# Optimization experiments

Hardware: AMD Instinct MI355X
Metric: run time of the kernel (lower is better)

Reference implementation:

```python
import jax, jax.numpy as jnp
import numpy as np

DIM = 1024
NUM_HEADS = 16
HEAD_DIM = DIM // NUM_HEADS


def setup_inputs() -> dict:
    key = jax.random.key(0)
    k_x, k_qkv, k_proj, k_b = jax.random.split(key, 4)
    B, N, P, C = 4, 96, 64, DIM
    x = jax.random.normal(k_x, (B, N, P, C), dtype=jnp.float32)
    # nn.Linear(dim, 3*dim, bias=False): store as (in, out) for x @ W
    s = 1.0 / np.sqrt(C)
    W_qkv = jax.random.uniform(k_qkv, (C, 3 * C), minval=-s, maxval=s, dtype=jnp.float32)
    W_proj = jax.random.uniform(k_proj, (C, C), minval=-s, maxval=s, dtype=jnp.float32)
    b_proj = jax.random.uniform(k_b, (C,), minval=-s, maxval=s, dtype=jnp.float32)
    return {"x": x, "W_qkv": W_qkv, "W_proj": W_proj, "b_proj": b_proj}


def reference(x, W_qkv, W_proj, b_proj):
    B, N, P, C = x.shape
    H, hd = NUM_HEADS, C // NUM_HEADS
    # qkv projection: (B,N,P,3C) -> (B,N,P,3,H,hd)
    qkv = (x @ W_qkv).reshape(B, N, P, 3, H, hd)
    # q,k: mean-pool over patches P -> (B,H,N,hd)
    q = qkv[..., 0, :, :].mean(axis=2).transpose(0, 2, 1, 3)
    k = qkv[..., 1, :, :].mean(axis=2).transpose(0, 2, 1, 3)
    # v keeps all patches: (B,N,P,H,hd) -> (B,H,N,hd,P) -> (B,H,N,hd*P)
    v = qkv[..., 2, :, :].transpose(0, 3, 1, 4, 2).reshape(B, H, N, hd * P)
    # SDPA with default scale 1/sqrt(q_last_dim) = 1/sqrt(hd)
    scores = jnp.einsum('bhnd,bhmd->bhnm', q, k) * (hd ** -0.5)
    attn = jax.nn.softmax(scores, axis=-1)
    out = jnp.einsum('bhnm,bhme->bhne', attn, v)  # e = hd*P
    # unflatten back to (B,N,P,C)
    out = out.reshape(B, H, N, hd, P).transpose(0, 2, 4, 1, 3).reshape(B, N, P, C)
    return out @ W_proj + b_proj
```

## Files before the change

kernel.cpp:

```cpp
#include <hip/hip_runtime.h>
#include <cstdint>
#include <cstddef>

#define PPP  64
#define CC   1024

typedef __attribute__((ext_vector_type(8))) short short8;
typedef __attribute__((ext_vector_type(4))) float floatx4;
typedef __attribute__((ext_vector_type(4))) unsigned short ushort4v;

__device__ inline float bf2f(unsigned short u) {
  union { unsigned int i; float f; } v; v.i = ((unsigned int)u) << 16; return v.f;
}
__device__ inline unsigned short f2bf(float f) {
  union { float f; unsigned int i; } v; v.f = f;
  unsigned int x = v.i;
  unsigned int r = (x + 0x7fffu + ((x >> 16) & 1u)) >> 16;
  return (unsigned short)r;
}

#define GLD16(gp, lp)                                                          \
  __builtin_amdgcn_global_load_lds(                                            \
      (const __attribute__((address_space(1))) void*)(gp),                     \
      (__attribute__((address_space(3))) void*)(lp), 16, 0, 0)

__global__ __launch_bounds__(256) void conv_mean(
    const float* __restrict__ x, unsigned short* __restrict__ xbf,
    unsigned short* __restrict__ xm) {
  int bn = blockIdx.x;
  int c4 = threadIdx.x * 4;
  const float* xp = x + (size_t)bn * (PPP * CC) + c4;
  unsigned short* xo = xbf + (size_t)bn * (PPP * CC) + c4;
  float4 s = {0.f, 0.f, 0.f, 0.f};
#pragma unroll 8
  for (int p = 0; p < PPP; ++p) {
    float4 v = *(const float4*)&xp[(size_t)p * CC];
    s.x += v.x; s.y += v.y; s.z += v.z; s.w += v.w;
    ushort4v pk;
    pk.x = f2bf(v.x); pk.y = f2bf(v.y); pk.z = f2bf(v.z); pk.w = f2bf(v.w);
    *(ushort4v*)&xo[(size_t)p * CC] = pk;
  }
  ushort4v pm;
  pm.x = f2bf(s.x * (1.0f / PPP)); pm.y = f2bf(s.y * (1.0f / PPP));
  pm.z = f2bf(s.z * (1.0f / PPP)); pm.w = f2bf(s.w * (1.0f / PPP));
  *(ushort4v*)&xm[(size_t)bn * CC + c4] = pm;
}

__global__ __launch_bounds__(256) void transpose_f32_bf16(
    const float* __restrict__ src, unsigned short* __restrict__ dst,
    int R, int Cc, int src_stride) {
  __shared__ unsigned short tile[32][33];
  int tc = blockIdx.x * 32, tr = blockIdx.y * 32;
  int tx = threadIdx.x & 31, ty = threadIdx.x >> 5;
  for (int yy = ty; yy < 32; yy += 8)
    tile[yy][tx] = f2bf(src[(size_t)(tr + yy) * src_stride + tc + tx]);
  __syncthreads();
  for (int yy = ty; yy < 32; yy += 8)
    dst[(size_t)(tc + yy) * R + tr + tx] = tile[tx][yy];
}

template <bool F32OUT, bool SWIZ>
__global__ __launch_bounds__(256) void gemm_bt(
    const unsigned short* __restrict__ A, const unsigned short* __restrict__ BT,
    void* __restrict__ Cout, const float* __restrict__ bias,
    int M, int N, int K, int nbx) {
  __shared__ unsigned short As[128 * 32];
  __shared__ unsigned short Bs[128 * 32];

  int bx, by;
  {
    int bid = blockIdx.x;
    if (SWIZ) {
      bx = (bid >> 3) & 7;
      by = (bid & 7) * (gridDim.x >> 6) + (bid >> 6);
    } else {
      bx = bid % nbx;
      by = bid / nbx;
    }
  }
  const int rowBase = by * 128;
  const int colBase = bx * 128;
  const int t = threadIdx.x;
  const int wave = t >> 6, lane = t & 63;
  const int qr = wave >> 1, qc = wave & 1;
  const int m16 = lane & 15, quad = lane >> 4;

  floatx4 acc[4][4];
#pragma unroll
  for (int i = 0; i < 4; ++i)
#pragma unroll
    for (int j = 0; j < 4; ++j) {
      acc[i][j][0] = 0.f; acc[i][j][1] = 0.f; acc[i][j][2] = 0.f; acc[i][j][3] = 0.f;
    }

  for (int k0 = 0; k0 < K; k0 += 32) {
    __syncthreads();
#pragma unroll
    for (int u = 0; u < 2; ++u) {
      int ch = (u * 4 + wave) * 64 + lane;
      int row = ch >> 2, c8 = (ch & 3) << 3;
      GLD16(&A [(size_t)(rowBase + row) * K + k0 + c8], &As[ch * 8]);
      GLD16(&BT[(size_t)(colBase + row) * K + k0 + c8], &Bs[ch * 8]);
    }
    __syncthreads();

    short8 af[4], bfr[4];
#pragma unroll
    for (int i = 0; i < 4; ++i)
      af[i] = *(const short8*)&As[(qr * 64 + i * 16 + m16) * 32 + quad * 8];
#pragma unroll
    for (int j = 0; j < 4; ++j)
      bfr[j] = *(const short8*)&Bs[(qc * 64 + j * 16 + m16) * 32 + quad * 8];
#pragma unroll
    for (int i = 0; i < 4; ++i)
#pragma unroll
      for (int j = 0; j < 4; ++j)
        acc[i][j] = __builtin_amdgcn_mfma_f32_16x16x32_bf16(af[i], bfr[j], acc[i][j], 0, 0, 0);
  }

  float bv[4];
#pragma unroll
  for (int j = 0; j < 4; ++j)
    bv[j] = bias ? bias[colBase + qc * 64 + j * 16 + m16] : 0.f;

#pragma unroll
  for (int i = 0; i < 4; ++i) {
    int row0 = rowBase + qr * 64 + i * 16 + quad * 4;
#pragma unroll
    for (int j = 0; j < 4; ++j) {
      int col = colBase + qc * 64 + j * 16 + m16;
#pragma unroll
      for (int r = 0; r < 4; ++r) {
        float f = acc[i][j][r] + bv[j];
        if (F32OUT)
          ((float*)Cout)[(size_t)(row0 + r) * N + col] = f;
        else
          ((unsigned short*)Cout)[(size_t)(row0 + r) * N + col] = f2bf(f);
      }
    }
  }
}

template <bool F32OUT>
__global__ __launch_bounds__(512, 2) void gemm_bt256(
    const unsigned short* __restrict__ A, const unsigned short* __restrict__ BT,
    void* __restrict__ Cout, const float* __restrict__ bias,
    int M, int N, int K) {
  __shared__ __attribute__((aligned(16))) unsigned short As[2][256 * 64];
  __shared__ __attribute__((aligned(16))) unsigned short Bs[3][256 * 64];

  const int nbx = N >> 8;
  int tid = (blockIdx.x & 7) * (gridDim.x >> 3) + (blockIdx.x >> 3);
  const int bx = tid % nbx, by = tid / nbx;
  const int rowBase = by * 256, colBase = bx * 256;

  const int t = threadIdx.x;
  const int wave = t >> 6, lane = t & 63;
  const int wr = wave >> 2, wc = wave & 3;
  const int m16 = lane & 15, quad = lane >> 4;
  const int sw7 = m16 & 7;

  const unsigned short* srcA[4];
  int offA[4];
#pragma unroll
  for (int u = 0; u < 4; ++u) {
    int c = u * 512 + t;
    int row = c >> 3, pch = c & 7;
    int l = pch ^ (row & 7);
    srcA[u] = A + (size_t)(rowBase + row) * K + l * 8;
    offA[u] = c * 8;
  }
  const unsigned short* srcB[2][2];
  int offB[2][2];
#pragma unroll
  for (int g = 0; g < 2; ++g)
#pragma unroll
    for (int u = 0; u < 2; ++u) {
      int i = u * 512 + t;
      int col = g * 32 + ((i >> 8) << 6) + ((i >> 3) & 31);
      int kcp = i & 7;
      int l = kcp ^ (col & 7);
      srcB[g][u] = BT + (size_t)(colBase + col) * K + l * 8;
      offB[g][u] = col * 64 + kcp * 8;
    }

  floatx4 acc[8][4];
#pragma unroll
  for (int i = 0; i < 8; ++i)
#pragma unroll
    for (int j = 0; j < 4; ++j) {
      acc[i][j][0] = 0.f; acc[i][j][1] = 0.f; acc[i][j][2] = 0.f; acc[i][j][3] = 0.f;
    }

  short8 ar[4][2];
  short8 br[2][2][2];

#define RD_A(buf, qa)                                                          \
  _Pragma("unroll") for (int i_ = 0; i_ < 4; ++i_)                             \
  _Pragma("unroll") for (int kh_ = 0; kh_ < 2; ++kh_)                          \
    ar[i_][kh_] = *(const short8*)&As[buf][                                    \
        (wr * 128 + (qa) * 64 + i_ * 16 + m16) * 64 +                          \
        (((kh_ * 4 + quad) ^ sw7) * 8)];
#define RD_B(buf, qb)                                                          \
  _Pragma("unroll") for (int j_ = 0; j_ < 2; ++j_)                             \
  _Pragma("unroll") for (int kh_ = 0; kh_ < 2; ++kh_)                          \
    br[qb][j_][kh_] = *(const short8*)&Bs[buf][                                \
        (wc * 64 + (qb) * 32 + j_ * 16 + m16) * 64 +                           \
        (((kh_ * 4 + quad) ^ sw7) * 8)];
#define MFMA_PH(qa, qb)                                                        \
  __builtin_amdgcn_s_setprio(1);                                               \
  _Pragma("unroll") for (int kh_ = 0; kh_ < 2; ++kh_)                          \
  _Pragma("unroll") for (int i_ = 0; i_ < 4; ++i_)                             \
  _Pragma("unroll") for (int j_ = 0; j_ < 2; ++j_)                             \
    acc[(qa) * 4 + i_][(qb) * 2 + j_] =                                        \
        __builtin_amdgcn_mfma_f32_16x16x32_bf16(                               \
            ar[i_][kh_], br[qb][j_][kh_], acc[(qa) * 4 + i_][(qb) * 2 + j_],   \
            0, 0, 0);                                                          \
  __builtin_amdgcn_s_setprio(0);
#define WAITV(n) asm volatile("s_waitcnt vmcnt(" #n ")" ::: "memory")
#define BARR() asm volatile("s_barrier" ::: "memory")
#define FEN() asm volatile("" ::: "memory")

  GLD16(srcB[0][0], &Bs[0][offB[0][0]]);
  GLD16(srcB[0][1], &Bs[0][offB[0][1]]); FEN();
  GLD16(srcB[1][0], &Bs[0][offB[1][0]]);
  GLD16(srcB[1][1], &Bs[0][offB[1][1]]); FEN();
  GLD16(srcA[0], &As[0][offA[0]]);
  GLD16(srcA[2], &As[0][offA[2]]); FEN();
  GLD16(srcA[1], &As[0][offA[1]]);
  GLD16(srcA[3], &As[0][offA[3]]); FEN();
  GLD16(srcB[0][0] + 64, &Bs[1][offB[0][0]]);
  GLD16(srcB[0][1] + 64, &Bs[1][offB[0][1]]); FEN();
  GLD16(srcB[1][0] + 64, &Bs[1][offB[1][0]]);
  GLD16(srcB[1][1] + 64, &Bs[1][offB[1][1]]); FEN();

  const int NT = K >> 6;
  int acur = 0, bcur = 0;
#pragma unroll 1
  for (int kt = 0; kt < NT - 1; ++kt) {
    const int anxt = acur ^ 1;
    const int bnx2 = (bcur >= 1) ? bcur - 1 : 2;
    const int koA = (kt + 1) << 6;
    const int koB = (kt + 2) << 6;
    const bool doB = (kt + 2) < NT;
    WAITV(4); BARR();
    RD_A(acur, 0);
    RD_B(bcur, 0);
    RD_B(bcur, 1);
    GLD16(srcA[0] + koA, &As[anxt][offA[0]]);
    GLD16(srcA[2] + koA, &As[anxt][offA[2]]); FEN();
    MFMA_PH(0, 0);
    GLD16(srcA[1] + koA, &As[anxt][offA[1]]);
    GLD16(srcA[3] + koA, &As[anxt][offA[3]]); FEN();
    MFMA_PH(0, 1);
    RD_A(acur, 1);
    if (doB) {
      GLD16(srcB[0][0] + koB, &Bs[bnx2][offB[0][0]]);
      GLD16(srcB[0][1] + koB, &Bs[bnx2][offB[0][1]]);
    }
    FEN();
    MFMA_PH(1, 0);
    if (doB) {
      GLD16(srcB[1][0] + koB, &Bs[bnx2][offB[1][0]]);
      GLD16(srcB[1][1] + koB, &Bs[bnx2][offB[1][1]]);
    }
    FEN();
    MFMA_PH(1, 1);
    acur = anxt; bcur = (bcur == 2) ? 0 : bcur + 1;
  }
  WAITV(0); BARR();
  RD_A(acur, 0); RD_B(bcur, 0); RD_B(bcur, 1);
  MFMA_PH(0, 0);
  MFMA_PH(0, 1);
  RD_A(acur, 1);
  MFMA_PH(1, 0);
  MFMA_PH(1, 1);

#undef RD_A
#undef RD_B
#undef MFMA_PH
#undef WAITV
#undef BARR
#undef FEN

  float bv[4];
#pragma unroll
  for (int jg = 0; jg < 4; ++jg)
    bv[jg] = bias ? bias[colBase + wc * 64 + jg * 16 + m16] : 0.f;

#pragma unroll
  for (int ig = 0; ig < 8; ++ig) {
    int row0 = rowBase + wr * 128 + ig * 16 + quad * 4;
#pragma unroll
    for (int jg = 0; jg < 4; ++jg) {
      int col = colBase + wc * 64 + jg * 16 + m16;
#pragma unroll
      for (int r = 0; r < 4; ++r) {
        float f = acc[ig][jg][r] + bv[jg];
        if (F32OUT)
          ((float*)Cout)[(size_t)(row0 + r) * N + col] = f;
        else
          ((unsigned short*)Cout)[(size_t)(row0 + r) * N + col] = f2bf(f);
      }
    }
  }
}

__global__ __launch_bounds__(128) void softmax_k(
    const float* __restrict__ qk, unsigned short* __restrict__ attn) {
  int bh = blockIdx.x;
  int b = bh >> 4, h = bh & 15;
  __shared__ float ks[96][64];
  __shared__ float sc[96][96];
  int t = threadIdx.x;
  for (int idx = t; idx < 96 * 64; idx += 128) {
    int n = idx >> 6, d = idx & 63;
    ks[n][d] = qk[(size_t)(b * 96 + n) * 2048 + 1024 + h * 64 + d];
  }
  __syncthreads();
  if (t < 96) {
    float qreg[64];
    const float* qrow = qk + (size_t)(b * 96 + t) * 2048 + h * 64;
#pragma unroll
    for (int d = 0; d < 64; ++d) qreg[d] = qrow[d];

    float mx = -1e30f;
    for (int m = 0; m < 96; ++m) {
      float s0 = 0.f, s1 = 0.f, s2 = 0.f, s3 = 0.f;
#pragma unroll
      for (int d = 0; d < 64; d += 4) {
        s0 += qreg[d + 0] * ks[m][d + 0];
        s1 += qreg[d + 1] * ks[m][d + 1];
        s2 += qreg[d + 2] * ks[m][d + 2];
        s3 += qreg[d + 3] * ks[m][d + 3];
      }
      float s = ((s0 + s1) + (s2 + s3)) * 0.125f;
      sc[m][t] = s;
      mx = fmaxf(mx, s);
    }
    float sum = 0.f;
    for (int m = 0; m < 96; ++m) {
      float e = __expf(sc[m][t] - mx);
      sc[m][t] = e;
      sum += e;
    }
    float inv = 1.0f / sum;
    size_t base = (size_t)(bh * 96 + t) * 96;
    for (int m = 0; m < 96; ++m) attn[base + m] = f2bf(sc[m][t] * inv);
  }
}

__global__ __launch_bounds__(256) void attn_apply_mfma(
    const unsigned short* __restrict__ attn, const unsigned short* __restrict__ V,
    unsigned short* __restrict__ out2) {
  const int bid = blockIdx.x;
  const int bh = bid >> 5, ct = bid & 31;
  const int b = bh >> 4;
  const int t = threadIdx.x;
  const int wave = t >> 6, lane = t & 63;
  const int m16 = lane & 15, quad = lane >> 4;

  const unsigned short* An = attn + (size_t)bh * 96 * 96;
  const int vb = b * 96 * 64 * CC;

  floatx4 acc[6][2];
#pragma unroll
  for (int i = 0; i < 6; ++i)
#pragma unroll
    for (int j = 0; j < 2; ++j) {
      acc[i][j][0] = 0.f; acc[i][j][1] = 0.f; acc[i][j][2] = 0.f; acc[i][j][3] = 0.f;
    }

  int p_[2], base_[2];
#pragma unroll
  for (int jj = 0; jj < 2; ++jj) {
    int colL = wave * 32 + jj * 16;
    int p = ct * 2 + (colL >> 6);
    int d = (colL & 63) + m16;
    p_[jj] = p;
    base_[jj] = vb + p * CC + ((bh & 15) * 64) + d;
  }

#pragma unroll
  for (int k0 = 0; k0 < 96; k0 += 32) {
    short8 af[6];
#pragma unroll
    for (int i = 0; i < 6; ++i)
      af[i] = *(const short8*)&An[(i * 16 + m16) * 96 + k0 + quad * 8];
#pragma unroll
    for (int jj = 0; jj < 2; ++jj) {
      short8 bfr;
#pragma unroll
      for (int j = 0; j < 8; ++j)
        bfr[j] = (short)V[(size_t)base_[jj] + (size_t)(k0 + quad * 8 + j) * (64 * CC)];
#pragma unroll
      for (int i = 0; i < 6; ++i)
        acc[i][jj] = __builtin_amdgcn_mfma_f32_16x16x32_bf16(af[i], bfr, acc[i][jj], 0, 0, 0);
    }
  }

#pragma unroll
  for (int jj = 0; jj < 2; ++jj) {
    int colL = wave * 32 + jj * 16;
    int d = (colL & 63) + m16;
    size_t obase = (size_t)(b * 96) * 64 * CC + (size_t)p_[jj] * CC + (bh & 15) * 64 + d;
#pragma unroll
    for (int i = 0; i < 6; ++i) {
#pragma unroll
      for (int r = 0; r < 4; ++r) {
        int n = i * 16 + quad * 4 + r;
        out2[obase + (size_t)n * (64 * CC)] = f2bf(acc[i][jj][r]);
      }
    }
  }
}

extern "C" void kernel_launch(void* const* d_in, const int* in_sizes, int n_in,
                              void* d_out, int out_size, void* d_ws, size_t ws_size,
                              hipStream_t stream) {
  const float* x      = (const float*)d_in[0];
  const float* W_qkv  = (const float*)d_in[1];
  const float* W_proj = (const float*)d_in[2];
  const float* b_proj = (const float*)d_in[3];
  float* out = (float*)d_out;

  char* w = (char*)d_ws;
  unsigned short* WqkvT = (unsigned short*)(w);
  unsigned short* WpT   = (unsigned short*)(w + 6291456);
  unsigned short* xm    = (unsigned short*)(w + 8388608);
  float*          qkbuf = (float*)(w + 9175040);
  unsigned short* attn  = (unsigned short*)(w + 12320768);
  unsigned short* out2w = (unsigned short*)(w + 13500416);
  unsigned short* xbf   = (unsigned short*)d_out;
  unsigned short* Vbuf  = (unsigned short*)((char*)d_out + 50331648);

  const bool fullws = ws_size >= (size_t)13500416 + 50331648;

  conv_mean<<<dim3(384), 256, 0, stream>>>(x, xbf, xm);

  transpose_f32_bf16<<<dim3(96, 32), 256, 0, stream>>>(W_qkv, WqkvT, 1024, 3072, 3072);
  transpose_f32_bf16<<<dim3(32, 32), 256, 0, stream>>>(W_proj, WpT, 1024, 1024, 1024);

  gemm_bt<true, false><<<dim3(48), 256, 0, stream>>>(
      xm, WqkvT, qkbuf, nullptr, 384, 2048, 1024, 16);

  softmax_k<<<dim3(64), 128, 0, stream>>>(qkbuf, attn);

  gemm_bt256<false><<<dim3(384), 512, 0, stream>>>(
      xbf, WqkvT + (size_t)2048 * 1024, Vbuf, nullptr, 24576, 1024, 1024);

  if (fullws) {
    attn_apply_mfma<<<dim3(2048), 256, 0, stream>>>(attn, Vbuf, out2w);
    gemm_bt256<true><<<dim3(384), 512, 0, stream>>>(
        out2w, WpT, out, b_proj, 24576, 1024, 1024);
  } else {
    for (int b = 0; b < 4; ++b) {
      attn_apply_mfma<<<dim3(512), 256, 0, stream>>>(
          attn + (size_t)b * 16 * 96 * 96,
          Vbuf + (size_t)b * 6144 * 1024,
          out2w);
      gemm_bt256<true><<<dim3(96), 512, 0, stream>>>(
          out2w, WpT, out + (size_t)b * 6144 * 1024, b_proj, 6144, 1024, 1024);
    }
  }
}
```

Before: 389.5 us.

## Stage V tile in swizzled LDS via async loads in attention-apply kernel

The attention-apply kernel now copies its 96x128 V tile into shared memory with 16-byte async global-to-LDS loads, using an XOR swizzle to cut bank conflicts. It previously gathered scalar 2-byte V elements straight from global memory with a large stride. All attention A fragments are now preloaded into registers, and the MFMA section is wrapped in s_setprio with a launch-bounds occupancy hint. This trades 24KB of LDS per block and extra registers for coalesced global traffic, and adds a full barrier before compute.

```diff
diff --git a/kernel.cpp b/kernel.cpp
--- a/kernel.cpp
+++ b/kernel.cpp
@@ -350,60 +350,75 @@
   }
 }
 
-__global__ __launch_bounds__(256) void attn_apply_mfma(
+__global__ __launch_bounds__(256, 2) void attn_apply_mfma(
     const unsigned short* __restrict__ attn, const unsigned short* __restrict__ V,
     unsigned short* __restrict__ out2) {
+  __shared__ __attribute__((aligned(16))) unsigned short Vt[96 * 128];
   const int bid = blockIdx.x;
   const int bh = bid >> 5, ct = bid & 31;
-  const int b = bh >> 4;
+  const int b = bh >> 4, h = bh & 15;
   const int t = threadIdx.x;
-  const int wave = t >> 6, lane = t & 63;
+  const int w = t >> 6, lane = t & 63;
   const int m16 = lane & 15, quad = lane >> 4;
+  const int p0 = ct * 2;
+
+#pragma unroll
+  for (int u = 0; u < 6; ++u) {
+    int c = u * 256 + t;
+    int m = c >> 4, pch = c & 15;
+    int l = pch ^ ((m >> 3) & 3);
+    const unsigned short* src =
+        V + (size_t)((b * 96 + m) * 64 + p0 + (l >> 3)) * CC + h * 64 + (l & 7) * 8;
+    GLD16(src, &Vt[c * 8]);
+  }
 
   const unsigned short* An = attn + (size_t)bh * 96 * 96;
-  const int vb = b * 96 * 64 * CC;
+  short8 a[6][3];
+#pragma unroll
+  for (int i = 0; i < 6; ++i)
+#pragma unroll
+    for (int kc = 0; kc < 3; ++kc)
+      a[i][kc] = *(const short8*)&An[(i * 16 + m16) * 96 + kc * 32 + quad * 8];
 
   floatx4 acc[6][2];
 #pragma unroll
   for (int i = 0; i < 6; ++i)
 #pragma unroll
-    for (int j = 0; j < 2; ++j) {
-      acc[i][j][0] = 0.f; acc[i][j][1] = 0.f; acc[i][j][2] = 0.f; acc[i][j][3] = 0.f;
-    }
-
-  int p_[2], base_[2];
+    for (int jj = 0; jj < 2; ++jj) {
+      acc[i][jj][0] = 0.f; acc[i][jj][1] = 0.f;
+      acc[i][jj][2] = 0.f; acc[i][jj][3] = 0.f;
+    }
+
+  asm volatile("s_waitcnt vmcnt(0)" ::: "memory");
+  __syncthreads();
+
+#pragma unroll
+  for (int kc = 0; kc < 3; ++kc) {
+    short8 bf[2];
+#pragma unroll
+    for (int jj = 0; jj < 2; ++jj) {
+      const int col = w * 32 + jj * 16 + m16;
+#pragma unroll
+      for (int jx = 0; jx < 8; ++jx) {
+        const int m = kc * 32 + quad * 8 + jx;
+        bf[jj][jx] = (short)Vt[m * 128 + (((col >> 3) ^ ((m >> 3) & 3)) << 3) + (col & 7)];
+      }
+    }
+    __builtin_amdgcn_s_setprio(1);
+#pragma unroll
+    for (int i = 0; i < 6; ++i)
+#pragma unroll
+      for (int jj = 0; jj < 2; ++jj)
+        acc[i][jj] = __builtin_amdgcn_mfma_f32_16x16x32_bf16(a[i][kc], bf[jj], acc[i][jj], 0, 0, 0);
+    __builtin_amdgcn_s_setprio(0);
+  }
+
 #pragma unroll
   for (int jj = 0; jj < 2; ++jj) {
-    int colL = wave * 32 + jj * 16;
-    int p = ct * 2 + (colL >> 6);
-    int d = (colL & 63) + m16;
-    p_[jj] = p;
-    base_[jj] = vb + p * CC + ((bh & 15) * 64) + d;
-  }
-
-#pragma unroll
-  for (int k0 = 0; k0 < 96; k0 += 32) {
-    short8 af[6];
-#pragma unroll
-    for (int i = 0; i < 6; ++i)
-      af[i] = *(const short8*)&An[(i * 16 + m16) * 96 + k0 + quad * 8];
-#pragma unroll
-    for (int jj = 0; jj < 2; ++jj) {
-      short8 bfr;
-#pragma unroll
-      for (int j = 0; j < 8; ++j)
-        bfr[j] = (short)V[(size_t)base_[jj] + (size_t)(k0 + quad * 8 + j) * (64 * CC)];
-#pragma unroll
-      for (int i = 0; i < 6; ++i)
-        acc[i][jj] = __builtin_amdgcn_mfma_f32_16x16x32_bf16(af[i], bfr, acc[i][jj], 0, 0, 0);
-    }
-  }
-
-#pragma unroll
-  for (int jj = 0; jj < 2; ++jj) {
-    int colL = wave * 32 + jj * 16;
-    int d = (colL & 63) + m16;
-    size_t obase = (size_t)(b * 96) * 64 * CC + (size_t)p_[jj] * CC + (bh & 15) * 64 + d;
+    const int colL = w * 32 + jj * 16;
+    const int p = p0 + (colL >> 6);
+    const int d = (colL & 63) + m16;
+    size_t obase = (size_t)(b * 96) * 64 * CC + (size_t)p * CC + h * 64 + d;
 #pragma unroll
     for (int i = 0; i < 6; ++i) {
 #pragma unroll
```

New measurement: 387.0 us. Within noise of the previous version (-0.6%).
